# Performance work log

Hardware: AMD Instinct MI355X
Metric: run time of the kernel (lower is better)

Reference implementation:

```python
import jax, jax.numpy as jnp
import numpy as np

N = 100000
E = 1600000
D_IN = 128
D_HID = 128
D_OUT = 128


def setup_inputs() -> dict:
    key = jax.random.key(0)
    ks = jax.random.split(key, 12)
    x = jax.random.normal(ks[0], (N, D_IN), dtype=jnp.float32)
    edge_index = jax.random.randint(ks[1], (2, E), 0, N, dtype=jnp.int32)
    def lin(k, fan_in, fan_out):
        s = 1.0 / np.sqrt(fan_in)
        return jax.random.uniform(k, (fan_in, fan_out), jnp.float32, -s, s)
    dims = [(D_IN, D_HID), (D_HID, D_HID), (D_HID, D_OUT)]
    inp = {"x": x, "edge_index": edge_index}
    for i, (fi, fo) in enumerate(dims):
        inp[f"Wl{i}"] = lin(ks[2 + 3 * i], fi, fo)
        inp[f"Wr{i}"] = lin(ks[3 + 3 * i], fi, fo)
        inp[f"b{i}"] = jnp.zeros((fo,), jnp.float32)
    return inp


def _sage_conv(h, row, col, Wl, Wr, b):
    # mean aggregation over incoming neighbors: out[i] = mean_{j->i} h[j]
    n = h.shape[0]
    agg = jax.ops.segment_sum(h[col], row, num_segments=n)  # [N, d]
    deg = jax.ops.segment_sum(jnp.ones_like(row, dtype=h.dtype), row, num_segments=n)
    agg = agg / jnp.maximum(deg, 1.0)[:, None]
    return agg @ Wl + b + h @ Wr


def reference(x, edge_index, Wl0, Wr0, b0, Wl1, Wr1, b1, Wl2, Wr2, b2):
    row, col = edge_index[0], edge_index[1]  # dst, src
    h1 = jax.nn.relu(_sage_conv(x, row, col, Wl0, Wr0, b0))   # dropout is no-op in eval
    h2 = jax.nn.relu(_sage_conv(h1, row, col, Wl1, Wr1, b1))
    h3 = jax.nn.relu(_sage_conv(h2, row, col, Wl2, Wr2, b2))
    return (h1, h2, h3)
```

## Files before the change

### kernel.cpp

```cpp
#include <hip/hip_runtime.h>

#define NN 100000
#define NE 1600000
#define DD 128
#define BM 64
#define NPB 256
#define NBUCK 391
#define ECHUNK 8192
#define NBLK_PART 196
#define CAP 8192
#define CVX_BLK 800
#define CVW_BLK 384

typedef __attribute__((ext_vector_type(2))) float f32x2;
typedef __attribute__((ext_vector_type(4))) float f32x4;
typedef __attribute__((ext_vector_type(8))) short bf16x8;

__device__ inline unsigned short f2bf(float f) {
    unsigned int x = __builtin_bit_cast(unsigned int, f);
    unsigned int r = x + 0x7fffu + ((x >> 16) & 1u);
    return (unsigned short)(r >> 16);
}
__device__ inline unsigned int packbf(float a, float b) {
    return (unsigned int)f2bf(a) | ((unsigned int)f2bf(b) << 16);
}
__device__ inline unsigned int pk_fp8x4(float a, float b, float c, float d) {
    int v = 0;
    v = __builtin_amdgcn_cvt_pk_fp8_f32(a, b, v, false);
    v = __builtin_amdgcn_cvt_pk_fp8_f32(c, d, v, true);
    return (unsigned int)v;
}
__device__ inline f32x2 upk_fp8_lo(unsigned int v) {
    return __builtin_amdgcn_cvt_pk_f32_fp8((int)v, false);
}
__device__ inline f32x2 upk_fp8_hi(unsigned int v) {
    return __builtin_amdgcn_cvt_pk_f32_fp8((int)v, true);
}


__global__ __launch_bounds__(256) void prep_kernel(
    const float* __restrict__ x, unsigned short* __restrict__ xb,
    unsigned int* __restrict__ xf8,
    const float* __restrict__ w0, const float* __restrict__ w1,
    const float* __restrict__ w2, const float* __restrict__ w3,
    const float* __restrict__ w4, const float* __restrict__ w5,
    unsigned short* __restrict__ wtall,
    const int* __restrict__ row, int* __restrict__ gcnt) {
    __shared__ int cnt[NBUCK];
    const int b = blockIdx.x;
    if (b < CVX_BLK) {
        int i = b * 256 + threadIdx.x;
        const int n4 = NN * DD / 4;
        for (; i < n4; i += CVX_BLK * 256) {
            float4 v = reinterpret_cast<const float4*>(x)[i];
            ushort4 o;
            o.x = f2bf(v.x); o.y = f2bf(v.y); o.z = f2bf(v.z); o.w = f2bf(v.w);
            reinterpret_cast<ushort4*>(xb)[i] = o;
            xf8[i] = pk_fp8x4(v.x, v.y, v.z, v.w);
        }
    } else if (b < CVX_BLK + CVW_BLK) {
        int t = (b - CVX_BLK) * 256 + threadIdx.x;
        int i = t >> 14;
        int r = t & 16383;
        const float* W = (i == 0) ? w0 : (i == 1) ? w1 : (i == 2) ? w2
                        : (i == 3) ? w3 : (i == 4) ? w4 : w5;
        int c = r >> 7, k = r & 127;
        wtall[t] = f2bf(W[k * DD + c]);
    } else {
        for (int i = threadIdx.x; i < NBUCK; i += 256) cnt[i] = 0;
        __syncthreads();
        int base = (b - CVX_BLK - CVW_BLK) * ECHUNK;
        int end = base + ECHUNK; if (end > NE) end = NE;
        for (int i = base + threadIdx.x; i < end; i += 256)
            atomicAdd(&cnt[row[i] >> 8], 1);
        __syncthreads();
        for (int i = threadIdx.x; i < NBUCK; i += 256) {
            int c = cnt[i];
            if (c) atomicAdd(&gcnt[i], c);
        }
    }
}


__global__ __launch_bounds__(512) void bucket_scan(const int* __restrict__ gcnt,
                                                   int* __restrict__ gbase) {
    __shared__ int sm[512];
    int t = threadIdx.x;
    sm[t] = (t < NBUCK) ? gcnt[t] : 0;
    __syncthreads();
    for (int off = 1; off < 512; off <<= 1) {
        int add = (t >= off) ? sm[t - off] : 0;
        __syncthreads();
        sm[t] += add;
        __syncthreads();
    }
    if (t < NBUCK) gbase[t + 1] = sm[t];
    if (t == 0) gbase[0] = 0;
}

__global__ __launch_bounds__(256) void bucket_scatter(const int* __restrict__ row,
                                                      const int* __restrict__ col,
                                                      const int* __restrict__ gbase,
                                                      int* __restrict__ gcursor,
                                                      unsigned int* __restrict__ ebuf) {
    __shared__ int cnt[NBUCK];
    __shared__ int base[NBUCK];
    for (int i = threadIdx.x; i < NBUCK; i += 256) cnt[i] = 0;
    __syncthreads();
    int cbase = blockIdx.x * ECHUNK;
    int cend = cbase + ECHUNK; if (cend > NE) cend = NE;
    for (int i = cbase + threadIdx.x; i < cend; i += 256)
        atomicAdd(&cnt[row[i] >> 8], 1);
    __syncthreads();
    for (int i = threadIdx.x; i < NBUCK; i += 256) {
        int c = cnt[i];
        cnt[i] = 0;
        base[i] = c ? (gbase[i] + atomicAdd(&gcursor[i], c)) : 0;
    }
    __syncthreads();
    for (int i = cbase + threadIdx.x; i < cend; i += 256) {
        int r = row[i], c = col[i];
        int b = r >> 8;
        int k = atomicAdd(&cnt[b], 1);
        ebuf[base[b] + k] = ((unsigned)c << 8) | ((unsigned)r & 255u);
    }
}

__global__ __launch_bounds__(256) void csr_build(const unsigned int* __restrict__ ebuf,
                                                 const int* __restrict__ gbase,
                                                 int* __restrict__ offs,
                                                 int* __restrict__ csr_col) {
    __shared__ int dcnt[NPB];
    __shared__ int doff[NPB];
    __shared__ int sm[NPB];
    __shared__ int stage[CAP];
    const int b = blockIdx.x;
    const int es = gbase[b], ee = gbase[b + 1];
    const int m = ee - es;
    const int t = threadIdx.x;
    const int nbase = b * NPB;

    dcnt[t] = 0;
    __syncthreads();
    for (int i = es + t; i < ee; i += 256) {
        int ln = (int)(ebuf[i] & 255u);
        atomicAdd(&dcnt[ln], 1);
    }
    __syncthreads();
    sm[t] = dcnt[t];
    __syncthreads();
    for (int off = 1; off < 256; off <<= 1) {
        int add = (t >= off) ? sm[t - off] : 0;
        __syncthreads();
        sm[t] += add;
        __syncthreads();
    }
    doff[t] = sm[t] - dcnt[t];
    int node = nbase + t;
    if (node < NN) offs[node + 1] = es + sm[t];
    if (b == 0 && t == 0) offs[0] = 0;
    dcnt[t] = 0;
    __syncthreads();

    if (m <= CAP) {
        for (int i = es + t; i < ee; i += 256) {
            unsigned e = ebuf[i];
            int ln = (int)(e & 255u);
            int k = atomicAdd(&dcnt[ln], 1);
            stage[doff[ln] + k] = (int)(e >> 8);
        }
        __syncthreads();
        for (int i = t; i < m; i += 256) csr_col[es + i] = stage[i];
    } else {
        for (int i = es + t; i < ee; i += 256) {
            unsigned e = ebuf[i];
            int ln = (int)(e & 255u);
            int k = atomicAdd(&dcnt[ln], 1);
            csr_col[es + doff[ln] + k] = (int)(e >> 8);
        }
    }
}


__global__ __launch_bounds__(256, 6) void fused_layer(
    const unsigned short* __restrict__ hb,
    const unsigned int* __restrict__ f8,
    const int* __restrict__ offs, const int* __restrict__ csr_col,
    const unsigned short* __restrict__ WlT, const unsigned short* __restrict__ WrT,
    const float* __restrict__ bias, float* __restrict__ out,
    unsigned short* __restrict__ hbn, unsigned int* __restrict__ f8n) {
    __shared__ uint4 smem4[1024];
    char* AldsB = (char*)smem4;
    const int row0 = blockIdx.x * BM;
    const int tid = threadIdx.x;
    const int w = tid >> 6, l = tid & 63;
    const int wr = w & 1, wc = w >> 1;
    const int lrow = l & 15, lg = l >> 4;

    bf16x8 aH[2][4];
#pragma unroll
    for (int m = 0; m < 2; ++m) {
        int gr = row0 + wr * 32 + m * 16 + lrow;
        if (gr >= NN) gr = NN - 1;
        const unsigned short* hrow = hb + (size_t)gr * DD;
#pragma unroll
        for (int kb = 0; kb < 4; ++kb)
            aH[m][kb] = *reinterpret_cast<const bf16x8*>(hrow + kb * 32 + lg * 8);
    }

    const int grp = tid >> 3, lane = tid & 7;
    const uint4* f84 = reinterpret_cast<const uint4*>(f8);
#pragma unroll
    for (int i = 0; i < 2; ++i) {
        const int rloc = grp * 2 + i;
        const int node = row0 + rloc;
        f32x2 a[8];
#pragma unroll
        for (int k = 0; k < 8; ++k) a[k] = (f32x2){0.f, 0.f};
        float inv = 0.0f;
        if (node < NN) {
            int s = offs[node], e = offs[node + 1];
            int p = s;
            for (; p + 8 <= e; p += 8) {
                uint4 v[8];
#pragma unroll
                for (int q = 0; q < 8; ++q)
                    v[q] = f84[(size_t)csr_col[p + q] * 8 + lane];
#pragma unroll
                for (int q = 0; q < 8; ++q) {
                    a[0] += upk_fp8_lo(v[q].x); a[1] += upk_fp8_hi(v[q].x);
                    a[2] += upk_fp8_lo(v[q].y); a[3] += upk_fp8_hi(v[q].y);
                    a[4] += upk_fp8_lo(v[q].z); a[5] += upk_fp8_hi(v[q].z);
                    a[6] += upk_fp8_lo(v[q].w); a[7] += upk_fp8_hi(v[q].w);
                }
            }
            for (; p < e; ++p) {
                uint4 v = f84[(size_t)csr_col[p] * 8 + lane];
                a[0] += upk_fp8_lo(v.x); a[1] += upk_fp8_hi(v.x);
                a[2] += upk_fp8_lo(v.y); a[3] += upk_fp8_hi(v.y);
                a[4] += upk_fp8_lo(v.z); a[5] += upk_fp8_hi(v.z);
                a[6] += upk_fp8_lo(v.w); a[7] += upk_fp8_hi(v.w);
            }
            inv = (e > s) ? (1.0f / (float)(e - s)) : 0.0f;
        }
        uint4 o0, o1;
        o0.x = packbf(a[0][0] * inv, a[0][1] * inv);
        o0.y = packbf(a[1][0] * inv, a[1][1] * inv);
        o0.z = packbf(a[2][0] * inv, a[2][1] * inv);
        o0.w = packbf(a[3][0] * inv, a[3][1] * inv);
        o1.x = packbf(a[4][0] * inv, a[4][1] * inv);
        o1.y = packbf(a[5][0] * inv, a[5][1] * inv);
        o1.z = packbf(a[6][0] * inv, a[6][1] * inv);
        o1.w = packbf(a[7][0] * inv, a[7][1] * inv);
        const int sw = (rloc & 7) << 4;
        const int rbase = rloc << 8;
        *reinterpret_cast<uint4*>(AldsB + rbase + ((lane * 32) ^ sw)) = o0;
        *reinterpret_cast<uint4*>(AldsB + rbase + ((lane * 32 + 16) ^ sw)) = o1;
    }
    __syncthreads();

    f32x4 acc[2][4];
#pragma unroll
    for (int m = 0; m < 2; ++m)
#pragma unroll
        for (int n = 0; n < 4; ++n) acc[m][n] = (f32x4){0.f, 0.f, 0.f, 0.f};

    float bv[4];
#pragma unroll
    for (int n = 0; n < 4; ++n) bv[n] = bias[wc * 64 + n * 16 + lrow];

#pragma unroll
    for (int kb = 0; kb < 4; ++kb) {
        const int kbyte = kb * 64 + lg * 16;
        bf16x8 aA[2];
#pragma unroll
        for (int m = 0; m < 2; ++m) {
            int rloc = wr * 32 + m * 16 + lrow;
            int off = (rloc << 8) + kbyte;
            off ^= (rloc & 7) << 4;
            aA[m] = *reinterpret_cast<const bf16x8*>(AldsB + off);
        }
        bf16x8 bL[4], bR[4];
#pragma unroll
        for (int n = 0; n < 4; ++n) {
            size_t woff = ((size_t)(wc * 64 + n * 16 + lrow) << 7) + kb * 32 + lg * 8;
            bL[n] = *reinterpret_cast<const bf16x8*>(WlT + woff);
            bR[n] = *reinterpret_cast<const bf16x8*>(WrT + woff);
        }
#pragma unroll
        for (int m = 0; m < 2; ++m)
#pragma unroll
            for (int n = 0; n < 4; ++n) {
                acc[m][n] = __builtin_amdgcn_mfma_f32_16x16x32_bf16(aA[m], bL[n], acc[m][n], 0, 0, 0);
                acc[m][n] = __builtin_amdgcn_mfma_f32_16x16x32_bf16(aH[m][kb], bR[n], acc[m][n], 0, 0, 0);
            }
    }

    __syncthreads();
    float* otile = (float*)smem4;
#pragma unroll
    for (int half = 0; half < 2; ++half) {
        if (wr == half) {
#pragma unroll
            for (int m = 0; m < 2; ++m) {
                int rb = m * 16 + lg * 4;
#pragma unroll
                for (int n = 0; n < 4; ++n) {
                    int c = wc * 64 + n * 16 + lrow;
#pragma unroll
                    for (int j = 0; j < 4; ++j)
                        otile[(rb + j) * DD + c] = fmaxf(acc[m][n][j] + bv[n], 0.0f);
                }
            }
        }
        __syncthreads();
        const f32x4* t4 = (const f32x4*)smem4;
#pragma unroll
        for (int it = 0; it < 4; ++it) {
            int idx = it * 256 + tid;
            int r = idx >> 5;
            int gr = row0 + half * 32 + r;
            if (gr < NN) {
                f32x4 v = t4[idx];
                __builtin_nontemporal_store(v, (f32x4*)out + (size_t)gr * 32 + (idx & 31));
                if (hbn) {
                    uint2 pk;
                    pk.x = packbf(v[0], v[1]);
                    pk.y = packbf(v[2], v[3]);
                    *((uint2*)hbn + (size_t)gr * 32 + (idx & 31)) = pk;
                    f8n[(size_t)gr * 32 + (idx & 31)] = pk_fp8x4(v[0], v[1], v[2], v[3]);
                }
            }
        }
        __syncthreads();
    }
}

extern "C" void kernel_launch(void* const* d_in, const int* in_sizes, int n_in,
                              void* d_out, int out_size, void* d_ws, size_t ws_size,
                              hipStream_t stream) {
    const float* x = (const float*)d_in[0];
    const int* ei = (const int*)d_in[1];
    const int* row = ei;
    const int* col = ei + NE;
    const float* Wl[3] = {(const float*)d_in[2], (const float*)d_in[5], (const float*)d_in[8]};
    const float* Wr[3] = {(const float*)d_in[3], (const float*)d_in[6], (const float*)d_in[9]};
    const float* bb[3] = {(const float*)d_in[4], (const float*)d_in[7], (const float*)d_in[10]};
    float* out = (float*)d_out;

    char* ws = (char*)d_ws;
    auto carve = [&](size_t bytes) {
        char* p = ws;
        ws += (bytes + 255) & ~(size_t)255;
        return p;
    };
    unsigned short* buf0 = (unsigned short*)carve((size_t)NN * DD * 2);
    unsigned short* buf1 = (unsigned short*)carve((size_t)NN * DD * 2);
    unsigned int* f8a = (unsigned int*)carve((size_t)NN * DD);
    unsigned int* f8b = (unsigned int*)carve((size_t)NN * DD);
    unsigned short* wtall = (unsigned short*)carve((size_t)6 * DD * DD * 2);
    int* gcnt    = (int*)carve((size_t)2 * NBUCK * sizeof(int));
    int* gcursor = gcnt + NBUCK;
    int* gbase   = (int*)carve((size_t)(NBUCK + 1) * sizeof(int));
    int* offs    = (int*)carve((size_t)(NN + 1) * sizeof(int));
    unsigned int* ebuf = (unsigned int*)carve((size_t)NE * sizeof(unsigned int));
    int* csr_col = (int*)carve((size_t)NE * sizeof(int));

    hipMemsetAsync(gcnt, 0, (size_t)2 * NBUCK * sizeof(int), stream);

    prep_kernel<<<CVX_BLK + CVW_BLK + NBLK_PART, 256, 0, stream>>>(
        x, buf0, f8a, Wl[0], Wr[0], Wl[1], Wr[1], Wl[2], Wr[2], wtall, row, gcnt);
    bucket_scan<<<1, 512, 0, stream>>>(gcnt, gbase);
    bucket_scatter<<<NBLK_PART, 256, 0, stream>>>(row, col, gbase, gcursor, ebuf);
    csr_build<<<NBUCK, 256, 0, stream>>>(ebuf, gbase, offs, csr_col);

    const int ngrid = (NN + BM - 1) / BM;

    unsigned short* hin = buf0;
    unsigned short* hout = buf1;
    unsigned int* f8in = f8a;
    unsigned int* f8out = f8b;
    for (int lyr = 0; lyr < 3; ++lyr) {
        float* o = out + (size_t)lyr * NN * DD;
        fused_layer<<<ngrid, 256, 0, stream>>>(
            hin, f8in, offs, csr_col,
            wtall + (size_t)2 * lyr * DD * DD, wtall + (size_t)(2 * lyr + 1) * DD * DD,
            bb[lyr], o,
            (lyr < 2) ? hout : (unsigned short*)nullptr,
            (lyr < 2) ? f8out : (unsigned int*)nullptr);
        unsigned short* t = hin; hin = hout; hout = t;
        unsigned int* t8 = f8in; f8in = f8out; f8out = t8;
    }
}
```

Before: 307.7 us.

## Fold bucket scan into scatter/CSR kernels and read fp32 x directly in layer 0

Removes the single-block bucket_scan launch by having bucket_scatter and csr_build each recompute the bucket prefix sum in shared memory from gcnt, and moves both kernels to 512 threads per block. The bf16 copy of x is no longer produced in prep; layer 0 instead loads fp32 x and converts it to bf16 in registers, which cuts a 25.6MB write and one launch. The cost is redundant scans in every block and twice the bytes read for the self-term rows in layer 0.

```diff
diff --git a/kernel.cpp b/kernel.cpp
--- a/kernel.cpp
+++ b/kernel.cpp
@@ -9,7 +9,7 @@
 #define ECHUNK 8192
 #define NBLK_PART 196
 #define CAP 8192
-#define CVX_BLK 800
+#define CVX_BLK 512
 #define CVW_BLK 384
 
 typedef __attribute__((ext_vector_type(2))) float f32x2;
@@ -39,8 +39,7 @@
 
 
 __global__ __launch_bounds__(256) void prep_kernel(
-    const float* __restrict__ x, unsigned short* __restrict__ xb,
-    unsigned int* __restrict__ xf8,
+    const float* __restrict__ x, unsigned int* __restrict__ xf8,
     const float* __restrict__ w0, const float* __restrict__ w1,
     const float* __restrict__ w2, const float* __restrict__ w3,
     const float* __restrict__ w4, const float* __restrict__ w5,
@@ -53,9 +52,6 @@
         const int n4 = NN * DD / 4;
         for (; i < n4; i += CVX_BLK * 256) {
             float4 v = reinterpret_cast<const float4*>(x)[i];
-            ushort4 o;
-            o.x = f2bf(v.x); o.y = f2bf(v.y); o.z = f2bf(v.z); o.w = f2bf(v.w);
-            reinterpret_cast<ushort4*>(xb)[i] = o;
             xf8[i] = pk_fp8x4(v.x, v.y, v.z, v.w);
         }
     } else if (b < CVX_BLK + CVW_BLK) {
@@ -82,43 +78,37 @@
 }
 
 
-__global__ __launch_bounds__(512) void bucket_scan(const int* __restrict__ gcnt,
-                                                   int* __restrict__ gbase) {
-    __shared__ int sm[512];
-    int t = threadIdx.x;
-    sm[t] = (t < NBUCK) ? gcnt[t] : 0;
-    __syncthreads();
-    for (int off = 1; off < 512; off <<= 1) {
-        int add = (t >= off) ? sm[t - off] : 0;
-        __syncthreads();
-        sm[t] += add;
-        __syncthreads();
-    }
-    if (t < NBUCK) gbase[t + 1] = sm[t];
-    if (t == 0) gbase[0] = 0;
-}
-
-__global__ __launch_bounds__(256) void bucket_scatter(const int* __restrict__ row,
+__global__ __launch_bounds__(512) void bucket_scatter(const int* __restrict__ row,
                                                       const int* __restrict__ col,
-                                                      const int* __restrict__ gbase,
+                                                      const int* __restrict__ gcnt,
                                                       int* __restrict__ gcursor,
                                                       unsigned int* __restrict__ ebuf) {
+    __shared__ int gb[512];
     __shared__ int cnt[NBUCK];
     __shared__ int base[NBUCK];
-    for (int i = threadIdx.x; i < NBUCK; i += 256) cnt[i] = 0;
-    __syncthreads();
+    const int t = threadIdx.x;
+    gb[t] = (t < NBUCK) ? gcnt[t] : 0;
+    if (t < NBUCK) cnt[t] = 0;
+    __syncthreads();
+    for (int off = 1; off < 512; off <<= 1) {
+        int add = (t >= off) ? gb[t - off] : 0;
+        __syncthreads();
+        gb[t] += add;
+        __syncthreads();
+    }
     int cbase = blockIdx.x * ECHUNK;
     int cend = cbase + ECHUNK; if (cend > NE) cend = NE;
-    for (int i = cbase + threadIdx.x; i < cend; i += 256)
+    for (int i = cbase + t; i < cend; i += 512)
         atomicAdd(&cnt[row[i] >> 8], 1);
     __syncthreads();
-    for (int i = threadIdx.x; i < NBUCK; i += 256) {
-        int c = cnt[i];
-        cnt[i] = 0;
-        base[i] = c ? (gbase[i] + atomicAdd(&gcursor[i], c)) : 0;
-    }
-    __syncthreads();
-    for (int i = cbase + threadIdx.x; i < cend; i += 256) {
+    if (t < NBUCK) {
+        int c = cnt[t];
+        cnt[t] = 0;
+        int g0 = t ? gb[t - 1] : 0;
+        base[t] = c ? (g0 + atomicAdd(&gcursor[t], c)) : 0;
+    }
+    __syncthreads();
+    for (int i = cbase + t; i < cend; i += 512) {
         int r = row[i], c = col[i];
         int b = r >> 8;
         int k = atomicAdd(&cnt[b], 1);
@@ -126,53 +116,66 @@
     }
 }
 
-__global__ __launch_bounds__(256) void csr_build(const unsigned int* __restrict__ ebuf,
-                                                 const int* __restrict__ gbase,
+__global__ __launch_bounds__(512) void csr_build(const unsigned int* __restrict__ ebuf,
+                                                 const int* __restrict__ gcnt,
                                                  int* __restrict__ offs,
                                                  int* __restrict__ csr_col) {
+    __shared__ int gb[512];
     __shared__ int dcnt[NPB];
     __shared__ int doff[NPB];
     __shared__ int sm[NPB];
     __shared__ int stage[CAP];
     const int b = blockIdx.x;
-    const int es = gbase[b], ee = gbase[b + 1];
-    const int m = ee - es;
     const int t = threadIdx.x;
     const int nbase = b * NPB;
 
-    dcnt[t] = 0;
-    __syncthreads();
-    for (int i = es + t; i < ee; i += 256) {
+    gb[t] = (t < NBUCK) ? gcnt[t] : 0;
+    if (t < NPB) dcnt[t] = 0;
+    __syncthreads();
+    for (int off = 1; off < 512; off <<= 1) {
+        int add = (t >= off) ? gb[t - off] : 0;
+        __syncthreads();
+        gb[t] += add;
+        __syncthreads();
+    }
+    const int es = b ? gb[b - 1] : 0;
+    const int ee = gb[b];
+    const int m = ee - es;
+
+    for (int i = es + t; i < ee; i += 512) {
         int ln = (int)(ebuf[i] & 255u);
         atomicAdd(&dcnt[ln], 1);
     }
     __syncthreads();
-    sm[t] = dcnt[t];
-    __syncthreads();
-    for (int off = 1; off < 256; off <<= 1) {
-        int add = (t >= off) ? sm[t - off] : 0;
-        __syncthreads();
-        sm[t] += add;
-        __syncthreads();
-    }
-    doff[t] = sm[t] - dcnt[t];
-    int node = nbase + t;
-    if (node < NN) offs[node + 1] = es + sm[t];
-    if (b == 0 && t == 0) offs[0] = 0;
-    dcnt[t] = 0;
+    if (t < NPB) sm[t] = dcnt[t];
+    __syncthreads();
+    for (int off = 1; off < NPB; off <<= 1) {
+        int add = 0;
+        if (t < NPB && t >= off) add = sm[t - off];
+        __syncthreads();
+        if (t < NPB) sm[t] += add;
+        __syncthreads();
+    }
+    if (t < NPB) {
+        doff[t] = sm[t] - dcnt[t];
+        int node = nbase + t;
+        if (node < NN) offs[node + 1] = es + sm[t];
+        if (b == 0 && t == 0) offs[0] = 0;
+        dcnt[t] = 0;
+    }
     __syncthreads();
 
     if (m <= CAP) {
-        for (int i = es + t; i < ee; i += 256) {
+        for (int i = es + t; i < ee; i += 512) {
             unsigned e = ebuf[i];
             int ln = (int)(e & 255u);
             int k = atomicAdd(&dcnt[ln], 1);
             stage[doff[ln] + k] = (int)(e >> 8);
         }
         __syncthreads();
-        for (int i = t; i < m; i += 256) csr_col[es + i] = stage[i];
+        for (int i = t; i < m; i += 512) csr_col[es + i] = stage[i];
     } else {
-        for (int i = es + t; i < ee; i += 256) {
+        for (int i = es + t; i < ee; i += 512) {
             unsigned e = ebuf[i];
             int ln = (int)(e & 255u);
             int k = atomicAdd(&dcnt[ln], 1);
@@ -182,7 +185,9 @@
 }
 
 
+template<bool L0>
 __global__ __launch_bounds__(256, 6) void fused_layer(
+    const float* __restrict__ hx,
     const unsigned short* __restrict__ hb,
     const unsigned int* __restrict__ f8,
     const int* __restrict__ offs, const int* __restrict__ csr_col,
@@ -202,10 +207,25 @@
     for (int m = 0; m < 2; ++m) {
         int gr = row0 + wr * 32 + m * 16 + lrow;
         if (gr >= NN) gr = NN - 1;
-        const unsigned short* hrow = hb + (size_t)gr * DD;
-#pragma unroll
-        for (int kb = 0; kb < 4; ++kb)
-            aH[m][kb] = *reinterpret_cast<const bf16x8*>(hrow + kb * 32 + lg * 8);
+        if (L0) {
+            const float* hrow = hx + (size_t)gr * DD;
+#pragma unroll
+            for (int kb = 0; kb < 4; ++kb) {
+                f32x4 v0 = *reinterpret_cast<const f32x4*>(hrow + kb * 32 + lg * 8);
+                f32x4 v1 = *reinterpret_cast<const f32x4*>(hrow + kb * 32 + lg * 8 + 4);
+                uint4 pk;
+                pk.x = packbf(v0[0], v0[1]);
+                pk.y = packbf(v0[2], v0[3]);
+                pk.z = packbf(v1[0], v1[1]);
+                pk.w = packbf(v1[2], v1[3]);
+                aH[m][kb] = __builtin_bit_cast(bf16x8, pk);
+            }
+        } else {
+            const unsigned short* hrow = hb + (size_t)gr * DD;
+#pragma unroll
+            for (int kb = 0; kb < 4; ++kb)
+                aH[m][kb] = *reinterpret_cast<const bf16x8*>(hrow + kb * 32 + lg * 8);
+        }
     }
 
     const int grp = tid >> 3, lane = tid & 7;
@@ -361,7 +381,6 @@
     unsigned short* wtall = (unsigned short*)carve((size_t)6 * DD * DD * 2);
     int* gcnt    = (int*)carve((size_t)2 * NBUCK * sizeof(int));
     int* gcursor = gcnt + NBUCK;
-    int* gbase   = (int*)carve((size_t)(NBUCK + 1) * sizeof(int));
     int* offs    = (int*)carve((size_t)(NN + 1) * sizeof(int));
     unsigned int* ebuf = (unsigned int*)carve((size_t)NE * sizeof(unsigned int));
     int* csr_col = (int*)carve((size_t)NE * sizeof(int));
@@ -369,26 +388,21 @@
     hipMemsetAsync(gcnt, 0, (size_t)2 * NBUCK * sizeof(int), stream);
 
     prep_kernel<<<CVX_BLK + CVW_BLK + NBLK_PART, 256, 0, stream>>>(
-        x, buf0, f8a, Wl[0], Wr[0], Wl[1], Wr[1], Wl[2], Wr[2], wtall, row, gcnt);
-    bucket_scan<<<1, 512, 0, stream>>>(gcnt, gbase);
-    bucket_scatter<<<NBLK_PART, 256, 0, stream>>>(row, col, gbase, gcursor, ebuf);
-    csr_build<<<NBUCK, 256, 0, stream>>>(ebuf, gbase, offs, csr_col);
+        x, f8a, Wl[0], Wr[0], Wl[1], Wr[1], Wl[2], Wr[2], wtall, row, gcnt);
+    bucket_scatter<<<NBLK_PART, 512, 0, stream>>>(row, col, gcnt, gcursor, ebuf);
+    csr_build<<<NBUCK, 512, 0, stream>>>(ebuf, gcnt, offs, csr_col);
 
     const int ngrid = (NN + BM - 1) / BM;
 
-    unsigned short* hin = buf0;
-    unsigned short* hout = buf1;
-    unsigned int* f8in = f8a;
-    unsigned int* f8out = f8b;
-    for (int lyr = 0; lyr < 3; ++lyr) {
-        float* o = out + (size_t)lyr * NN * DD;
-        fused_layer<<<ngrid, 256, 0, stream>>>(
-            hin, f8in, offs, csr_col,
-            wtall + (size_t)2 * lyr * DD * DD, wtall + (size_t)(2 * lyr + 1) * DD * DD,
-            bb[lyr], o,
-            (lyr < 2) ? hout : (unsigned short*)nullptr,
-            (lyr < 2) ? f8out : (unsigned int*)nullptr);
-        unsigned short* t = hin; hin = hout; hout = t;
-        unsigned int* t8 = f8in; f8in = f8out; f8out = t8;
-    }
-}
+    fused_layer<true><<<ngrid, 256, 0, stream>>>(
+        x, (const unsigned short*)nullptr, f8a, offs, csr_col,
+        wtall, wtall + (size_t)DD * DD, bb[0], out, buf0, f8b);
+    fused_layer<false><<<ngrid, 256, 0, stream>>>(
+        (const float*)nullptr, buf0, f8b, offs, csr_col,
+        wtall + (size_t)2 * DD * DD, wtall + (size_t)3 * DD * DD, bb[1],
+        out + (size_t)NN * DD, buf1, f8a);
+    fused_layer<false><<<ngrid, 256, 0, stream>>>(
+        (const float*)nullptr, buf1, f8a, offs, csr_col,
+        wtall + (size_t)4 * DD * DD, wtall + (size_t)5 * DD * DD, bb[2],
+        out + (size_t)2 * NN * DD, (unsigned short*)nullptr, (unsigned int*)nullptr);
+}
```

Result: slower. 362.0 us (+17.6%).

## Balance neighbor aggregation by splitting block edges evenly across thread groups

Applied to the files above, without the earlier changes.

Replaces per-node gather (each 8-lane group owning two nodes) with an edge-balanced split: the block's contiguous CSR edge range is divided evenly across 32 groups, each finds its starting row by binary search and flushes partial sums into a 32 KB fp32 LDS tile with shared-memory atomics. Mean scaling and bf16 packing move into the MFMA A-operand load, and the epilogue writes the whole 64-row tile in one pass. This targets load imbalance from varying node degrees, at the cost of LDS atomics, larger LDS use, and reduced occupancy (launch bound lowered from 6 to 4 blocks).

```diff
diff --git a/kernel.cpp b/kernel.cpp
--- a/kernel.cpp
+++ b/kernel.cpp
@@ -182,15 +182,15 @@
 }
 
 
-__global__ __launch_bounds__(256, 6) void fused_layer(
+__global__ __launch_bounds__(256, 4) void fused_layer(
     const unsigned short* __restrict__ hb,
     const unsigned int* __restrict__ f8,
     const int* __restrict__ offs, const int* __restrict__ csr_col,
     const unsigned short* __restrict__ WlT, const unsigned short* __restrict__ WrT,
     const float* __restrict__ bias, float* __restrict__ out,
     unsigned short* __restrict__ hbn, unsigned int* __restrict__ f8n) {
-    __shared__ uint4 smem4[1024];
-    char* AldsB = (char*)smem4;
+    __shared__ float accf[BM * DD];
+    __shared__ int offsL[BM + 1];
     const int row0 = blockIdx.x * BM;
     const int tid = threadIdx.x;
     const int w = tid >> 6, l = tid & 63;
@@ -208,56 +208,93 @@
             aH[m][kb] = *reinterpret_cast<const bf16x8*>(hrow + kb * 32 + lg * 8);
     }
 
+    if (tid <= BM) {
+        int n = row0 + tid;
+        offsL[tid] = offs[n < NN ? n : NN];
+    }
+    {
+        f32x4 z = {0.f, 0.f, 0.f, 0.f};
+#pragma unroll
+        for (int i = 0; i < 8; ++i)
+            *reinterpret_cast<f32x4*>(accf + (i * 256 + tid) * 4) = z;
+    }
+    __syncthreads();
+
+    const int eb = offsL[0], ee = offsL[BM];
+    const int mtot = ee - eb;
     const int grp = tid >> 3, lane = tid & 7;
     const uint4* f84 = reinterpret_cast<const uint4*>(f8);
-#pragma unroll
-    for (int i = 0; i < 2; ++i) {
-        const int rloc = grp * 2 + i;
-        const int node = row0 + rloc;
-        f32x2 a[8];
-#pragma unroll
-        for (int k = 0; k < 8; ++k) a[k] = (f32x2){0.f, 0.f};
-        float inv = 0.0f;
-        if (node < NN) {
-            int s = offs[node], e = offs[node + 1];
-            int p = s;
-            for (; p + 8 <= e; p += 8) {
+    if (mtot > 0) {
+        const int chunk = (mtot + 31) >> 5;
+        int p0 = eb + grp * chunk;
+        int p1 = p0 + chunk; if (p1 > ee) p1 = ee;
+        if (p0 < p1) {
+            int lo = 0, hi = BM - 1;
+            while (lo < hi) {
+                int mid = (lo + hi + 1) >> 1;
+                if (offsL[mid] <= p0) lo = mid; else hi = mid - 1;
+            }
+            int r = lo;
+            int rEnd = offsL[r + 1];
+            f32x2 a[8];
+#pragma unroll
+            for (int k = 0; k < 8; ++k) a[k] = (f32x2){0.f, 0.f};
+            bool dirty = false;
+
+            for (int p = p0; p < p1; p += 8) {
                 uint4 v[8];
 #pragma unroll
-                for (int q = 0; q < 8; ++q)
-                    v[q] = f84[(size_t)csr_col[p + q] * 8 + lane];
-#pragma unroll
                 for (int q = 0; q < 8; ++q) {
+                    int idx = p + q; if (idx > p1 - 1) idx = p1 - 1;
+                    v[q] = f84[(size_t)csr_col[idx] * 8 + lane];
+                }
+#pragma unroll
+                for (int q = 0; q < 8; ++q) {
+                    int idx = p + q;
+                    if (idx >= p1) break;
+                    if (idx >= rEnd) {
+                        if (dirty) {
+                            float* rowp = accf + r * DD;
+                            int swz = (r & 7) << 3;
+#pragma unroll
+                            for (int k = 0; k < 8; ++k) {
+                                int d = (lane * 16 + k * 2) ^ swz;
+                                atomicAdd(rowp + d, a[k][0]);
+                                atomicAdd(rowp + d + 1, a[k][1]);
+                                a[k] = (f32x2){0.f, 0.f};
+                            }
+                            dirty = false;
+                        }
+                        do { ++r; rEnd = offsL[r + 1]; } while (idx >= rEnd);
+                    }
                     a[0] += upk_fp8_lo(v[q].x); a[1] += upk_fp8_hi(v[q].x);
                     a[2] += upk_fp8_lo(v[q].y); a[3] += upk_fp8_hi(v[q].y);
                     a[4] += upk_fp8_lo(v[q].z); a[5] += upk_fp8_hi(v[q].z);
                     a[6] += upk_fp8_lo(v[q].w); a[7] += upk_fp8_hi(v[q].w);
+                    dirty = true;
                 }
             }
-            for (; p < e; ++p) {
-                uint4 v = f84[(size_t)csr_col[p] * 8 + lane];
-                a[0] += upk_fp8_lo(v.x); a[1] += upk_fp8_hi(v.x);
-                a[2] += upk_fp8_lo(v.y); a[3] += upk_fp8_hi(v.y);
-                a[4] += upk_fp8_lo(v.z); a[5] += upk_fp8_hi(v.z);
-                a[6] += upk_fp8_lo(v.w); a[7] += upk_fp8_hi(v.w);
+            if (dirty) {
+                float* rowp = accf + r * DD;
+                int swz = (r & 7) << 3;
+#pragma unroll
+                for (int k = 0; k < 8; ++k) {
+                    int d = (lane * 16 + k * 2) ^ swz;
+                    atomicAdd(rowp + d, a[k][0]);
+                    atomicAdd(rowp + d + 1, a[k][1]);
+                }
             }
-            inv = (e > s) ? (1.0f / (float)(e - s)) : 0.0f;
-        }
-        uint4 o0, o1;
-        o0.x = packbf(a[0][0] * inv, a[0][1] * inv);
-        o0.y = packbf(a[1][0] * inv, a[1][1] * inv);
-        o0.z = packbf(a[2][0] * inv, a[2][1] * inv);
-        o0.w = packbf(a[3][0] * inv, a[3][1] * inv);
-        o1.x = packbf(a[4][0] * inv, a[4][1] * inv);
-        o1.y = packbf(a[5][0] * inv, a[5][1] * inv);
-        o1.z = packbf(a[6][0] * inv, a[6][1] * inv);
-        o1.w = packbf(a[7][0] * inv, a[7][1] * inv);
-        const int sw = (rloc & 7) << 4;
-        const int rbase = rloc << 8;
-        *reinterpret_cast<uint4*>(AldsB + rbase + ((lane * 32) ^ sw)) = o0;
-        *reinterpret_cast<uint4*>(AldsB + rbase + ((lane * 32 + 16) ^ sw)) = o1;
-    }
-    __syncthreads();
+        }
+    }
+    __syncthreads();
+
+    float invm[2];
+#pragma unroll
+    for (int m = 0; m < 2; ++m) {
+        int rloc = wr * 32 + m * 16 + lrow;
+        int deg = offsL[rloc + 1] - offsL[rloc];
+        invm[m] = (deg > 0) ? (1.0f / (float)deg) : 0.0f;
+    }
 
     f32x4 acc[2][4];
 #pragma unroll
@@ -271,14 +308,22 @@
 
 #pragma unroll
     for (int kb = 0; kb < 4; ++kb) {
-        const int kbyte = kb * 64 + lg * 16;
         bf16x8 aA[2];
 #pragma unroll
         for (int m = 0; m < 2; ++m) {
             int rloc = wr * 32 + m * 16 + lrow;
-            int off = (rloc << 8) + kbyte;
-            off ^= (rloc & 7) << 4;
-            aA[m] = *reinterpret_cast<const bf16x8*>(AldsB + off);
+            int k = kb * 32 + lg * 8;
+            int d = k ^ ((rloc & 7) << 3);
+            const float* src = accf + rloc * DD + d;
+            f32x4 u0 = *reinterpret_cast<const f32x4*>(src);
+            f32x4 u1 = *reinterpret_cast<const f32x4*>(src + 4);
+            float inv = invm[m];
+            uint4 pk;
+            pk.x = packbf(u0[0] * inv, u0[1] * inv);
+            pk.y = packbf(u0[2] * inv, u0[3] * inv);
+            pk.z = packbf(u1[0] * inv, u1[1] * inv);
+            pk.w = packbf(u1[2] * inv, u1[3] * inv);
+            aA[m] = __builtin_bit_cast(bf16x8, pk);
         }
         bf16x8 bL[4], bR[4];
 #pragma unroll
@@ -297,42 +342,36 @@
     }
 
     __syncthreads();
-    float* otile = (float*)smem4;
-#pragma unroll
-    for (int half = 0; half < 2; ++half) {
-        if (wr == half) {
-#pragma unroll
-            for (int m = 0; m < 2; ++m) {
-                int rb = m * 16 + lg * 4;
-#pragma unroll
-                for (int n = 0; n < 4; ++n) {
-                    int c = wc * 64 + n * 16 + lrow;
-#pragma unroll
-                    for (int j = 0; j < 4; ++j)
-                        otile[(rb + j) * DD + c] = fmaxf(acc[m][n][j] + bv[n], 0.0f);
-                }
+    float* otile = accf;
+#pragma unroll
+    for (int m = 0; m < 2; ++m) {
+        int rb = wr * 32 + m * 16 + lg * 4;
+#pragma unroll
+        for (int n = 0; n < 4; ++n) {
+            int c = wc * 64 + n * 16 + lrow;
+#pragma unroll
+            for (int j = 0; j < 4; ++j)
+                otile[(rb + j) * DD + c] = fmaxf(acc[m][n][j] + bv[n], 0.0f);
+        }
+    }
+    __syncthreads();
+    const f32x4* t4 = (const f32x4*)accf;
+#pragma unroll
+    for (int it = 0; it < 8; ++it) {
+        int idx = it * 256 + tid;
+        int r = idx >> 5;
+        int gr = row0 + r;
+        if (gr < NN) {
+            f32x4 v = t4[idx];
+            __builtin_nontemporal_store(v, (f32x4*)out + (size_t)gr * 32 + (idx & 31));
+            if (hbn) {
+                uint2 pk;
+                pk.x = packbf(v[0], v[1]);
+                pk.y = packbf(v[2], v[3]);
+                *((uint2*)hbn + (size_t)gr * 32 + (idx & 31)) = pk;
+                f8n[(size_t)gr * 32 + (idx & 31)] = pk_fp8x4(v[0], v[1], v[2], v[3]);
             }
         }
-        __syncthreads();
-        const f32x4* t4 = (const f32x4*)smem4;
-#pragma unroll
-        for (int it = 0; it < 4; ++it) {
-            int idx = it * 256 + tid;
-            int r = idx >> 5;
-            int gr = row0 + half * 32 + r;
-            if (gr < NN) {
-                f32x4 v = t4[idx];
-                __builtin_nontemporal_store(v, (f32x4*)out + (size_t)gr * 32 + (idx & 31));
-                if (hbn) {
-                    uint2 pk;
-                    pk.x = packbf(v[0], v[1]);
-                    pk.y = packbf(v[2], v[3]);
-                    *((uint2*)hbn + (size_t)gr * 32 + (idx & 31)) = pk;
-                    f8n[(size_t)gr * 32 + (idx & 31)] = pk_fp8x4(v[0], v[1], v[2], v[3]);
-                }
-            }
-        }
-        __syncthreads();
     }
 }
 
```

Measured after the change: 447.5 us. 1.45x slower.
